# Kernel tuning notes

Hardware: AMD Instinct MI355X
Metric: run time of the kernel (lower is better)

Reference implementation:

```python
import jax, jax.numpy as jnp
import numpy as np
from jax import lax

TAU = 20.0
DT = 1.0
V_TH = 1.0
V_RESET = 0.0


def lif_spike(x):
    # Heaviside spike (surrogate gradient only matters for backward)
    return (x > 0).astype(x.dtype)


def setup_inputs() -> dict:
    key = jax.random.key(0)
    k1, k2, k3 = jax.random.split(key, 3)
    T, B, IN, OUT = 100, 256, 1024, 1024
    input_spikes = jax.random.uniform(k1, (T, B, IN), dtype=jnp.float32)
    # nn.Linear default init: U(-1/sqrt(in), 1/sqrt(in)) scale; randn*0.03 is fine for a numeric baseline
    W = jax.random.normal(k2, (OUT, IN), dtype=jnp.float32) * (1.0 / np.sqrt(IN))
    b = jax.random.normal(k3, (OUT,), dtype=jnp.float32) * 0.01
    return {"input_spikes": input_spikes, "W": W, "b": b}


def reference(input_spikes, W, b):
    T, B, _ = input_spikes.shape
    OUT = W.shape[0]
    # Precompute all input currents with one big GEMM: [T,B,out]
    I_all = jnp.einsum('tbi,oi->tbo', input_spikes, W) + b

    def step(v, I):
        v = v + (-v / TAU + I) * DT          # leaky integration
        s = lif_spike(v - V_TH)              # threshold
        v = jnp.where(s > 0, V_RESET, v)     # reset on spike
        return v, s

    v0 = jnp.zeros((B, OUT), dtype=input_spikes.dtype)
    _, spikes = lax.scan(step, v0, I_all)
    return spikes  # [T, B, out]
```

## Files before the change

kernel.cpp:

```cpp
#include <hip/hip_runtime.h>


constexpr int kT   = 100;
constexpr int kB   = 256;
constexpr int kIn  = 1024;
constexpr int kOut = 1024;
constexpr int kM   = kT * kB;

constexpr int BM = 128;
constexpr int BN = 128;
constexpr int BK = 16;
constexpr int NT = kIn / BK;

__global__ __launch_bounds__(256, 4)
void gemm_f32(const float* __restrict__ A,
              const float* __restrict__ W,
              const float* __restrict__ bias,
              float* __restrict__ I)
{
    __shared__ float As[2][BK * BM];
    __shared__ float Ws[2][BK * BN];

    const int tid = threadIdx.x;
    const int m0  = blockIdx.y * BM;
    const int n0  = blockIdx.x * BN;

    const int tc = tid & 15;
    const int tr = tid >> 4;

    const int pw0 = (((2 * tc    ) ^ ((2 * tc    ) >> 2)) & 31) * 4;
    const int pw1 = (((2 * tc + 1) ^ ((2 * tc + 1) >> 2)) & 31) * 4;

    const int sr  = tid >> 1;
    const int sc0 = (tid & 1) * 8;
    const float* Arow = A + (size_t)(m0 + sr) * kIn + sc0;
    const float* Wrow = W + (size_t)(n0 + sr) * kIn + sc0;
    const int wslot = ((((sr >> 2) ^ (sr >> 4)) & 31) * 4) + (sr & 3);

    float4 la[2], lw[2];
#pragma unroll
    for (int i = 0; i < 2; ++i) {
        la[i] = *reinterpret_cast<const float4*>(Arow + i * 4);
        lw[i] = *reinterpret_cast<const float4*>(Wrow + i * 4);
    }

    float acc[8][8];
#pragma unroll
    for (int j = 0; j < 8; ++j)
#pragma unroll
        for (int l = 0; l < 8; ++l) acc[j][l] = 0.0f;

    for (int t = 0; t < NT; ++t) {
        float* Ab = As[t & 1];
        float* Wb = Ws[t & 1];

#pragma unroll
        for (int i = 0; i < 2; ++i) {
            const float* pa = reinterpret_cast<const float*>(&la[i]);
            const float* pw = reinterpret_cast<const float*>(&lw[i]);
#pragma unroll
            for (int kk = 0; kk < 4; ++kk) {
                const int k = sc0 + i * 4 + kk;
                Ab[k * BM + sr]    = pa[kk];
                Wb[k * BN + wslot] = pw[kk];
            }
        }

        __syncthreads();

        if (t + 1 < NT) {
            const int kn = (t + 1) * BK;
#pragma unroll
            for (int i = 0; i < 2; ++i) {
                la[i] = *reinterpret_cast<const float4*>(Arow + kn + i * 4);
                lw[i] = *reinterpret_cast<const float4*>(Wrow + kn + i * 4);
            }
        }

#pragma unroll 4
        for (int k = 0; k < BK; ++k) {
            const float4 a0 = *reinterpret_cast<const float4*>(&Ab[k * BM + tr * 8]);
            const float4 a1 = *reinterpret_cast<const float4*>(&Ab[k * BM + tr * 8 + 4]);
            const float4 w0 = *reinterpret_cast<const float4*>(&Wb[k * BN + pw0]);
            const float4 w1 = *reinterpret_cast<const float4*>(&Wb[k * BN + pw1]);
            const float a[8] = {a0.x, a0.y, a0.z, a0.w, a1.x, a1.y, a1.z, a1.w};
            const float w[8] = {w0.x, w0.y, w0.z, w0.w, w1.x, w1.y, w1.z, w1.w};
#pragma unroll
            for (int j = 0; j < 8; ++j)
#pragma unroll
                for (int l = 0; l < 8; ++l)
                    acc[j][l] = fmaf(a[j], w[l], acc[j][l]);
        }
    }

#pragma unroll
    for (int j = 0; j < 8; ++j) {
        const int m = m0 + tr * 8 + j;
#pragma unroll
        for (int h = 0; h < 2; ++h) {
            const int n = n0 + tc * 8 + h * 4;
            float4 o4;
            o4.x = acc[j][h * 4 + 0] + bias[n + 0];
            o4.y = acc[j][h * 4 + 1] + bias[n + 1];
            o4.z = acc[j][h * 4 + 2] + bias[n + 2];
            o4.w = acc[j][h * 4 + 3] + bias[n + 3];
            *reinterpret_cast<float4*>(&I[(size_t)m * kOut + n]) = o4;
        }
    }
}

__global__ __launch_bounds__(256)
void lif_scan_f32(const float* Iin, float* out)
{
    const int idx4 = (blockIdx.x * blockDim.x + threadIdx.x) * 4;
    if (idx4 >= kB * kOut) return;

    float v0 = 0.0f, v1 = 0.0f, v2 = 0.0f, v3 = 0.0f;
    for (int t = 0; t < kT; ++t) {
        const size_t off = (size_t)t * (kB * kOut) + idx4;
        const float4 Iv = *reinterpret_cast<const float4*>(&Iin[off]);
        float4 s4;

        { const float t1 = v0 / 20.0f; const float u = Iv.x - t1; v0 = v0 + u;
          const bool s = (v0 > 1.0f); s4.x = s ? 1.0f : 0.0f; if (s) v0 = 0.0f; }
        { const float t1 = v1 / 20.0f; const float u = Iv.y - t1; v1 = v1 + u;
          const bool s = (v1 > 1.0f); s4.y = s ? 1.0f : 0.0f; if (s) v1 = 0.0f; }
        { const float t1 = v2 / 20.0f; const float u = Iv.z - t1; v2 = v2 + u;
          const bool s = (v2 > 1.0f); s4.z = s ? 1.0f : 0.0f; if (s) v2 = 0.0f; }
        { const float t1 = v3 / 20.0f; const float u = Iv.w - t1; v3 = v3 + u;
          const bool s = (v3 > 1.0f); s4.w = s ? 1.0f : 0.0f; if (s) v3 = 0.0f; }

        *reinterpret_cast<float4*>(&out[off]) = s4;
    }
}

extern "C" void kernel_launch(void* const* d_in, const int* in_sizes, int n_in,
                              void* d_out, int out_size, void* d_ws, size_t ws_size,
                              hipStream_t stream) {
    const float* spikes = (const float*)d_in[0];
    const float* W      = (const float*)d_in[1];
    const float* bias   = (const float*)d_in[2];
    float* out = (float*)d_out;

    const size_t iBytes = (size_t)kM * kOut * sizeof(float);
    dim3 grid(kOut / BN, kM / BM);

    float* Ibuf = (ws_size >= iBytes && d_ws != nullptr) ? (float*)d_ws : out;
    gemm_f32<<<grid, 256, 0, stream>>>(spikes, W, bias, Ibuf);
    lif_scan_f32<<<(kB * kOut) / (256 * 4), 256, 0, stream>>>(Ibuf, out);
}
```

Measured before the change: 672.2 us.

## Load A operand directly from global memory instead of staging through LDS

Removes the shared-memory tile for the input-spike matrix. Each thread now reads its 8 A rows straight from global memory as float2 pairs inside the inner loop, while W stays staged through LDS. This cuts LDS usage and the A store/load traffic. In exchange, each thread issues many uncoalesced, strided global loads with no software prefetch, relying on cache hits since 16 threads share the same rows.

```diff
diff --git a/kernel.cpp b/kernel.cpp
--- a/kernel.cpp
+++ b/kernel.cpp
@@ -18,7 +18,6 @@
               const float* __restrict__ bias,
               float* __restrict__ I)
 {
-    __shared__ float As[2][BK * BM];
     __shared__ float Ws[2][BK * BN];
 
     const int tid = threadIdx.x;
@@ -33,16 +32,13 @@
 
     const int sr  = tid >> 1;
     const int sc0 = (tid & 1) * 8;
-    const float* Arow = A + (size_t)(m0 + sr) * kIn + sc0;
     const float* Wrow = W + (size_t)(n0 + sr) * kIn + sc0;
     const int wslot = ((((sr >> 2) ^ (sr >> 4)) & 31) * 4) + (sr & 3);
 
-    float4 la[2], lw[2];
-#pragma unroll
-    for (int i = 0; i < 2; ++i) {
-        la[i] = *reinterpret_cast<const float4*>(Arow + i * 4);
-        lw[i] = *reinterpret_cast<const float4*>(Wrow + i * 4);
-    }
+    const float* Abase = A + (size_t)(m0 + tr * 8) * kIn;
+
+    float4 lw0 = *reinterpret_cast<const float4*>(Wrow);
+    float4 lw1 = *reinterpret_cast<const float4*>(Wrow + 4);
 
     float acc[8][8];
 #pragma unroll
@@ -51,45 +47,47 @@
         for (int l = 0; l < 8; ++l) acc[j][l] = 0.0f;
 
     for (int t = 0; t < NT; ++t) {
-        float* Ab = As[t & 1];
         float* Wb = Ws[t & 1];
 
-#pragma unroll
-        for (int i = 0; i < 2; ++i) {
-            const float* pa = reinterpret_cast<const float*>(&la[i]);
-            const float* pw = reinterpret_cast<const float*>(&lw[i]);
+        {
+            const float* p0 = reinterpret_cast<const float*>(&lw0);
+            const float* p1 = reinterpret_cast<const float*>(&lw1);
 #pragma unroll
             for (int kk = 0; kk < 4; ++kk) {
-                const int k = sc0 + i * 4 + kk;
-                Ab[k * BM + sr]    = pa[kk];
-                Wb[k * BN + wslot] = pw[kk];
+                Wb[(sc0 + kk)     * BN + wslot] = p0[kk];
+                Wb[(sc0 + 4 + kk) * BN + wslot] = p1[kk];
             }
         }
 
         __syncthreads();
 
         if (t + 1 < NT) {
-            const int kn = (t + 1) * BK;
-#pragma unroll
-            for (int i = 0; i < 2; ++i) {
-                la[i] = *reinterpret_cast<const float4*>(Arow + kn + i * 4);
-                lw[i] = *reinterpret_cast<const float4*>(Wrow + kn + i * 4);
-            }
+            lw0 = *reinterpret_cast<const float4*>(Wrow + (t + 1) * BK);
+            lw1 = *reinterpret_cast<const float4*>(Wrow + (t + 1) * BK + 4);
         }
 
-#pragma unroll 4
-        for (int k = 0; k < BK; ++k) {
-            const float4 a0 = *reinterpret_cast<const float4*>(&Ab[k * BM + tr * 8]);
-            const float4 a1 = *reinterpret_cast<const float4*>(&Ab[k * BM + tr * 8 + 4]);
-            const float4 w0 = *reinterpret_cast<const float4*>(&Wb[k * BN + pw0]);
-            const float4 w1 = *reinterpret_cast<const float4*>(&Wb[k * BN + pw1]);
-            const float a[8] = {a0.x, a0.y, a0.z, a0.w, a1.x, a1.y, a1.z, a1.w};
-            const float w[8] = {w0.x, w0.y, w0.z, w0.w, w1.x, w1.y, w1.z, w1.w};
+#pragma unroll
+        for (int p = 0; p < 8; ++p) {
+            const int k2 = t * BK + 2 * p;
+            float2 a2[8];
 #pragma unroll
             for (int j = 0; j < 8; ++j)
+                a2[j] = *reinterpret_cast<const float2*>(Abase + (size_t)j * kIn + k2);
+
 #pragma unroll
-                for (int l = 0; l < 8; ++l)
-                    acc[j][l] = fmaf(a[j], w[l], acc[j][l]);
+            for (int kk = 0; kk < 2; ++kk) {
+                const int k = 2 * p + kk;
+                const float4 w0 = *reinterpret_cast<const float4*>(&Wb[k * BN + pw0]);
+                const float4 w1 = *reinterpret_cast<const float4*>(&Wb[k * BN + pw1]);
+                const float w[8] = {w0.x, w0.y, w0.z, w0.w, w1.x, w1.y, w1.z, w1.w};
+#pragma unroll
+                for (int j = 0; j < 8; ++j) {
+                    const float aj = kk ? a2[j].y : a2[j].x;
+#pragma unroll
+                    for (int l = 0; l < 8; ++l)
+                        acc[j][l] = fmaf(aj, w[l], acc[j][l]);
+                }
+            }
         }
     }
 
```

Result: slower. 1.321 ms (+96.5%).
